# Kernel optimization log

Measured on AMD Instinct MI355X. Metric: run time of the kernel, lower is better.

## Reference

```python
import jax, jax.numpy as jnp
import numpy as np

EPS = 1e-5
HEADS, DK, DV = 8, 32, 64  # active_num_heads, active_key_dim, key_dim*attn_ratio


def _bn(x, g, b, m, v):
    # eval-mode BatchNorm2d over channel axis 1
    s = g * jax.lax.rsqrt(v + EPS)
    return x * s[None, :, None, None] + (b - m * s)[None, :, None, None]


def _bn_params(key, n):
    k1, k2, k3, k4 = jax.random.split(key, 4)
    gamma = 1.0 + 0.1 * jax.random.normal(k1, (n,), jnp.float32)
    beta = 0.1 * jax.random.normal(k2, (n,), jnp.float32)
    mean = 0.1 * jax.random.normal(k3, (n,), jnp.float32)
    var = jax.random.uniform(k4, (n,), jnp.float32, 0.5, 1.5)
    return gamma, beta, mean, var


def setup_inputs() -> dict:
    key = jax.random.key(0)
    ks = jax.random.split(key, 9)
    B, C, H, W = 8, 384, 32, 32
    Cqk, Cv = DK * HEADS, DV * HEADS  # 256, 512
    x = jax.random.normal(ks[0], (B, C, H, W), jnp.float32)
    w_q = jax.random.normal(ks[1], (Cqk, C), jnp.float32) / np.sqrt(C)
    w_k = jax.random.normal(ks[2], (Cqk, C), jnp.float32) / np.sqrt(C)
    w_v = jax.random.normal(ks[3], (Cv, C), jnp.float32) / np.sqrt(C)
    w_proj = jax.random.normal(ks[4], (C, Cv), jnp.float32) / np.sqrt(Cv)
    g_q, b_q, m_q, var_q = _bn_params(ks[5], Cqk)
    g_k, b_k, m_k, var_k = _bn_params(ks[6], Cqk)
    g_v, b_v, m_v, var_v = _bn_params(ks[7], Cv)
    g_p, b_p, m_p, var_p = _bn_params(ks[8], C)
    return dict(x=x, w_q=w_q, g_q=g_q, b_q=b_q, m_q=m_q, var_q=var_q,
                w_k=w_k, g_k=g_k, b_k=b_k, m_k=m_k, var_k=var_k,
                w_v=w_v, g_v=g_v, b_v=b_v, m_v=m_v, var_v=var_v,
                w_proj=w_proj, g_p=g_p, b_p=b_p, m_p=m_p, var_p=var_p)


def reference(x, w_q, g_q, b_q, m_q, var_q,
              w_k, g_k, b_k, m_k, var_k,
              w_v, g_v, b_v, m_v, var_v,
              w_proj, g_p, b_p, m_p, var_p):
    B, C, H, W = x.shape
    N = H * W
    # active config == max config, so dynamic index gathers are identity
    q = _bn(jnp.einsum('oc,bchw->bohw', w_q, x), g_q, b_q, m_q, var_q)
    k = _bn(jnp.einsum('oc,bchw->bohw', w_k, x), g_k, b_k, m_k, var_k)
    v = _bn(jnp.einsum('oc,bchw->bohw', w_v, x), g_v, b_v, m_v, var_v)
    q = q.reshape(B, HEADS, DK, N).transpose(0, 1, 3, 2)   # b h n d
    k = k.reshape(B, HEADS, DK, N)                          # b h d m
    v = v.reshape(B, HEADS, DV, N).transpose(0, 1, 3, 2)   # b h m e
    # NOTE: original forward does NOT apply self.scale
    attn = jax.nn.softmax(jnp.einsum('bhnd,bhdm->bhnm', q, k), axis=-1)
    out = jnp.einsum('bhnm,bhme->bhne', attn, v)
    out = out.transpose(0, 1, 3, 2).reshape(B, HEADS * DV, H, W)
    out = jax.nn.relu(out)
    out = _bn(jnp.einsum('oc,bchw->bohw', w_proj, out), g_p, b_p, m_p, var_p)
    return out
```

## Files before the change

### kernel.cpp

```cpp
#include <hip/hip_runtime.h>
#include <hip/hip_bf16.h>

#define DEVI __device__ __forceinline__

typedef __attribute__((ext_vector_type(8))) short s16x8;
typedef __attribute__((ext_vector_type(4))) short s16x4;
typedef __attribute__((ext_vector_type(4))) float f32x4;

#define LOG2E 1.4426950408889634f

DEVI short f2bs(float f) {
    unsigned u = __builtin_bit_cast(unsigned, f);
    unsigned r = (u + 0x7fffu + ((u >> 16) & 1u)) >> 16;
    return (short)r;
}

DEVI f32x4 mfma16(s16x8 a, s16x8 b, f32x4 c) {
    return __builtin_amdgcn_mfma_f32_16x16x32_bf16(a, b, c, 0, 0, 0);
}

DEVI void gl_lds16(const short* g, short* l) {
    __builtin_amdgcn_global_load_lds(
        (const __attribute__((address_space(1))) unsigned*)(const void*)g,
        (__attribute__((address_space(3))) unsigned*)(void*)l, 16, 0, 0);
}

__global__ __launch_bounds__(256) void k_prep_x(const float* __restrict__ x,
                                                short* __restrict__ xt) {
    __shared__ float tile[32][33];
    const int ct = blockIdx.x, nt = blockIdx.y, b = blockIdx.z;
    const int t = threadIdx.x;
    {
        const int j = t & 31, i0 = (t >> 5) * 4;
        const float* src = x + ((size_t)b * 384 + (size_t)ct * 32) * 1024 + nt * 32;
#pragma unroll
        for (int ii = 0; ii < 4; ++ii)
            tile[i0 + ii][j] = src[(size_t)(i0 + ii) * 1024 + j];
    }
    __syncthreads();
    {
        const int ii = t & 31, j0 = (t >> 5) * 4;
        short* dst = xt + ((size_t)b * 1024 + (size_t)nt * 32) * 384 + ct * 32;
#pragma unroll
        for (int jj = 0; jj < 4; ++jj)
            dst[(size_t)(j0 + jj) * 384 + ii] = f2bs(tile[ii][j0 + jj]);
    }
}

__global__ __launch_bounds__(256) void k_prep_w(
    const float* __restrict__ wq, const float* __restrict__ wk,
    const float* __restrict__ wv, const float* __restrict__ wp,
    short* __restrict__ wqkv, short* __restrict__ wpb,
    const float* gq, const float* bq, const float* mq, const float* vq,
    const float* gk, const float* bk, const float* mk, const float* vk,
    const float* gv, const float* bv, const float* mv, const float* vv,
    const float* gp, const float* bp, const float* mp, const float* vp,
    float* s_qkv, float* t_qkv, float* s_p, float* t_p) {
    int i = blockIdx.x * 256 + threadIdx.x;
    if (i < 1024) {
        const float *g, *bb, *mm, *vv_;
        int o = i;
        float post = 1.0f;
        if (i < 256)      { g = gq; bb = bq; mm = mq; vv_ = vq; post = LOG2E; }
        else if (i < 512) { g = gk; bb = bk; mm = mk; vv_ = vk; o = i - 256; }
        else              { g = gv; bb = bv; mm = mv; vv_ = vv; o = i - 512; }
        float s = g[o] * rsqrtf(vv_[o] + 1e-5f);
        s_qkv[i] = s * post;
        t_qkv[i] = (bb[o] - mm[o] * s) * post;
        if (i < 384) {
            float sp = gp[i] * rsqrtf(vp[i] + 1e-5f);
            s_p[i] = sp;
            t_p[i] = bp[i] - mp[i] * sp;
        }
    }
    const int NQKV = 1024 * 384;
    if (i < NQKV) {
        int o = i / 384;
        float v;
        if (o < 256)      v = wq[i];
        else if (o < 512) v = wk[i - 256 * 384];
        else              v = wv[i - 512 * 384];
        wqkv[i] = f2bs(v);
    } else {
        int j = i - NQKV;
        if (j < 384 * 512) wpb[j] = f2bs(wp[j]);
    }
}

__global__ __launch_bounds__(256, 2) void k_gemm_qkv(
    const short* __restrict__ wqkv, const short* __restrict__ xt,
    const float* __restrict__ s_qkv, const float* __restrict__ t_qkv,
    short* __restrict__ Qw, short* __restrict__ Kw, short* __restrict__ Vw) {
    __shared__ short AB[2][8192];
    const int t = threadIdx.x, lane = t & 63, w = t >> 6;
    const int g = lane >> 4, l15 = lane & 15;
    const int wr = w >> 1, wc = w & 1;
    const int jb = blockIdx.x, mb = blockIdx.y;

    const int cr = t >> 2, cu = t & 3;
    const int cperm = 8 * (cu ^ (cr & 3));
    const short* gA0 = wqkv + (size_t)(mb * 128 + cr) * 384 + cperm;
    const short* gA1 = wqkv + (size_t)(mb * 128 + cr + 64) * 384 + cperm;
    const short* gB0 = xt + (size_t)((size_t)jb * 128 + cr) * 384 + cperm;
    const short* gB1 = xt + (size_t)((size_t)jb * 128 + cr + 64) * 384 + cperm;

    f32x4 acc[4][4];
#pragma unroll
    for (int mi = 0; mi < 4; ++mi)
#pragma unroll
        for (int ni = 0; ni < 4; ++ni) acc[mi][ni] = f32x4{0.f, 0.f, 0.f, 0.f};

    const int kcol = 8 * (g ^ (l15 & 3));

    auto stage = [&](int ks, int buf) {
        short* base = AB[buf];
        gl_lds16(gA0 + ks * 32, base + t * 8);
        gl_lds16(gA1 + ks * 32, base + (t + 256) * 8);
        gl_lds16(gB0 + ks * 32, base + 4096 + t * 8);
        gl_lds16(gB1 + ks * 32, base + 4096 + (t + 256) * 8);
    };

    stage(0, 0);
    __syncthreads();

    for (int ks = 0; ks < 12; ++ks) {
        if (ks < 11) stage(ks + 1, (ks + 1) & 1);
        const short* base = AB[ks & 1];
        s16x8 a[4], b[4];
#pragma unroll
        for (int mi = 0; mi < 4; ++mi)
            a[mi] = *(const s16x8*)(base + (64 * wr + 16 * mi + l15) * 32 + kcol);
#pragma unroll
        for (int ni = 0; ni < 4; ++ni)
            b[ni] = *(const s16x8*)(base + 4096 + (64 * wc + 16 * ni + l15) * 32 + kcol);
#pragma unroll
        for (int mi = 0; mi < 4; ++mi)
#pragma unroll
            for (int ni = 0; ni < 4; ++ni)
                acc[mi][ni] = mfma16(a[mi], b[ni], acc[mi][ni]);
        __syncthreads();
    }

    const int m_base = mb * 128 + 64 * wr;
    const int j_base = jb * 128 + 64 * wc;
#pragma unroll
    for (int mi = 0; mi < 4; ++mi) {
        const int o0 = m_base + 16 * mi;
#pragma unroll
        for (int ni = 0; ni < 4; ++ni) {
            const int j = j_base + 16 * ni + l15;
            const int bb = j >> 10, n = j & 1023;
            if (o0 < 512) {
                const int o = o0 + 4 * g;
                const int isK = o0 >= 256;
                const int o2 = o - (isK ? 256 : 0);
                const int h = o2 >> 5, d0 = o2 & 31;
                s16x4 ov;
#pragma unroll
                for (int r = 0; r < 4; ++r)
                    ov[r] = f2bs(acc[mi][ni][r] * s_qkv[o + r] + t_qkv[o + r]);
                short* dst = (isK ? Kw : Qw) + (((size_t)bb * 8 + h) * 1024 + n) * 32 + d0;
                *(s16x4*)dst = ov;
            } else {
#pragma unroll
                for (int r = 0; r < 4; ++r) {
                    const int o = o0 + 4 * g + r;
                    float val = acc[mi][ni][r] * s_qkv[o] + t_qkv[o];
                    const int o2 = o - 512;
                    const int h = o2 >> 6, e = o2 & 63;
                    Vw[(((size_t)bb * 8 + h) * 64 + e) * 1024 + n] = f2bs(val);
                }
            }
        }
    }
}

__global__ __launch_bounds__(256, 2) void k_attn(const short* __restrict__ Qw,
                                                 const short* __restrict__ Kw,
                                                 const short* __restrict__ Vw,
                                                 short* __restrict__ Ow) {
    __shared__ short KV[2][6144];
    const int t = threadIdx.x, lane = t & 63, w = t >> 6;
    const int g = lane >> 4, l15 = lane & 15;
    const int low3 = blockIdx.x & 7;
    const int mid = blockIdx.x >> 3;
    const int rb = mid & 7;
    const int bh = ((mid >> 3) << 3) | low3;
    const int n_base = rb * 128 + w * 32;
    const short* Qb = Qw + (size_t)bh * (1024 * 32);
    const short* Kb = Kw + (size_t)bh * (1024 * 32);
    const short* Vb = Vw + (size_t)bh * (64 * 1024);

    s16x8 qf[2];
#pragma unroll
    for (int i = 0; i < 2; ++i)
        qf[i] = *(const s16x8*)(Qb + (size_t)(n_base + 16 * i + l15) * 32 + 8 * g);

    const int skr = t >> 2, sku = t & 3;
    const short* gK = Kb + (size_t)skr * 32 + 8 * (sku ^ (skr & 3));
    const int v0r = t >> 3, vu = t & 7;
    const short* gV0 = Vb + (size_t)v0r * 1024 + 8 * (vu ^ (v0r & 7));
    const short* gV1 = Vb + (size_t)(v0r + 32) * 1024 + 8 * (vu ^ ((v0r + 32) & 7));

    f32x4 oacc[2][4];
#pragma unroll
    for (int niq = 0; niq < 2; ++niq)
#pragma unroll
        for (int ei = 0; ei < 4; ++ei) oacc[niq][ei] = f32x4{0.f, 0.f, 0.f, 0.f};
    float l_part[2] = {0.f, 0.f};

    const int krow = 8 * (l15 >> 2) + (l15 & 3);
    const int kcol = 8 * (g ^ (l15 & 3));

    auto stage = [&](int m0, int buf) {
        short* base = KV[buf];
        gl_lds16(gK + m0 * 32, base + t * 8);
        gl_lds16(gV0 + m0, base + 2048 + t * 8);
        gl_lds16(gV1 + m0, base + 2048 + (t + 256) * 8);
    };

    stage(0, 0);
    __syncthreads();

    for (int mt = 0; mt < 16; ++mt) {
        if (mt < 15) stage((mt + 1) * 64, (mt + 1) & 1);
        const short* base = KV[mt & 1];
        s16x8 kf[4];
        kf[0] = *(const s16x8*)(base + (krow + 0) * 32 + kcol);
        kf[1] = *(const s16x8*)(base + (krow + 4) * 32 + kcol);
        kf[2] = *(const s16x8*)(base + (krow + 32) * 32 + kcol);
        kf[3] = *(const s16x8*)(base + (krow + 36) * 32 + kcol);
        s16x8 vb[2][4];
#pragma unroll
        for (int ki = 0; ki < 2; ++ki)
#pragma unroll
            for (int ei = 0; ei < 4; ++ei) {
                const int row = 16 * ei + l15;
                vb[ki][ei] = *(const s16x8*)(base + 2048 + row * 64 +
                                             8 * ((4 * ki + g) ^ (row & 7)));
            }
        f32x4 st[4][2];
#pragma unroll
        for (int mik = 0; mik < 4; ++mik)
#pragma unroll
            for (int niq = 0; niq < 2; ++niq)
                st[mik][niq] = mfma16(kf[mik], qf[niq], f32x4{0.f, 0.f, 0.f, 0.f});
        s16x4 pk[4][2];
#pragma unroll
        for (int mik = 0; mik < 4; ++mik)
#pragma unroll
            for (int niq = 0; niq < 2; ++niq) {
                float p[4];
#pragma unroll
                for (int r = 0; r < 4; ++r) p[r] = __builtin_amdgcn_exp2f(st[mik][niq][r]);
                l_part[niq] += (p[0] + p[1]) + (p[2] + p[3]);
#pragma unroll
                for (int r = 0; r < 4; ++r) pk[mik][niq][r] = f2bs(p[r]);
            }
#pragma unroll
        for (int ki = 0; ki < 2; ++ki)
#pragma unroll
            for (int niq = 0; niq < 2; ++niq) {
                s16x8 pb = __builtin_shufflevector(pk[2 * ki][niq], pk[2 * ki + 1][niq],
                                                   0, 1, 2, 3, 4, 5, 6, 7);
#pragma unroll
                for (int ei = 0; ei < 4; ++ei)
                    oacc[niq][ei] = mfma16(vb[ki][ei], pb, oacc[niq][ei]);
            }
        __syncthreads();
    }

    float li[2];
#pragma unroll
    for (int niq = 0; niq < 2; ++niq) {
        float s = l_part[niq];
        s += __shfl_xor(s, 16, 64);
        s += __shfl_xor(s, 32, 64);
        li[niq] = __builtin_amdgcn_rcpf(s);
    }
    const int b = bh >> 3, h = bh & 7;
#pragma unroll
    for (int niq = 0; niq < 2; ++niq) {
        const int n = n_base + 16 * niq + l15;
#pragma unroll
        for (int ei = 0; ei < 4; ++ei) {
            s16x4 ov;
#pragma unroll
            for (int r = 0; r < 4; ++r)
                ov[r] = f2bs(fmaxf(oacc[niq][ei][r] * li[niq], 0.f));
            *(s16x4*)(Ow + ((size_t)b * 1024 + n) * 512 + h * 64 + 16 * ei + 4 * g) = ov;
        }
    }
}

__global__ __launch_bounds__(256, 3) void k_proj(const short* __restrict__ wpb,
                                                 const short* __restrict__ Ow,
                                                 const float* __restrict__ s_p,
                                                 const float* __restrict__ t_p,
                                                 float* __restrict__ out) {
    __shared__ short AB[2][4096];
    const int t = threadIdx.x, lane = t & 63, w = t >> 6;
    const int g = lane >> 4, l15 = lane & 15;
    const int wr = w >> 1, wc = w & 1;
    const int jb = blockIdx.x, mb = blockIdx.y;

    const int cr = t >> 2, cu = t & 3;
    const int cperm = 8 * (cu ^ (cr & 3));
    const short* gA = wpb + (size_t)(mb * 64 + cr) * 512 + cperm;
    const short* gB = Ow + (size_t)((size_t)jb * 64 + cr) * 512 + cperm;

    f32x4 acc[2][2];
#pragma unroll
    for (int mi = 0; mi < 2; ++mi)
#pragma unroll
        for (int ni = 0; ni < 2; ++ni) acc[mi][ni] = f32x4{0.f, 0.f, 0.f, 0.f};

    const int kcol = 8 * (g ^ (l15 & 3));

    auto stage = [&](int ks, int buf) {
        short* base = AB[buf];
        gl_lds16(gA + ks * 32, base + t * 8);
        gl_lds16(gB + ks * 32, base + 2048 + t * 8);
    };

    stage(0, 0);
    __syncthreads();

    for (int ks = 0; ks < 16; ++ks) {
        if (ks < 15) stage(ks + 1, (ks + 1) & 1);
        const short* base = AB[ks & 1];
        s16x8 a[2], b[2];
#pragma unroll
        for (int mi = 0; mi < 2; ++mi)
            a[mi] = *(const s16x8*)(base + (32 * wr + 16 * mi + l15) * 32 + kcol);
#pragma unroll
        for (int ni = 0; ni < 2; ++ni)
            b[ni] = *(const s16x8*)(base + 2048 + (32 * wc + 16 * ni + l15) * 32 + kcol);
#pragma unroll
        for (int mi = 0; mi < 2; ++mi)
#pragma unroll
            for (int ni = 0; ni < 2; ++ni)
                acc[mi][ni] = mfma16(a[mi], b[ni], acc[mi][ni]);
        __syncthreads();
    }

    const int m_base = mb * 64 + 32 * wr;
    const int j_base = jb * 64 + 32 * wc;
#pragma unroll
    for (int mi = 0; mi < 2; ++mi) {
#pragma unroll
        for (int ni = 0; ni < 2; ++ni) {
            const int j = j_base + 16 * ni + l15;
            const int bb = j >> 10, n = j & 1023;
#pragma unroll
            for (int r = 0; r < 4; ++r) {
                const int c = m_base + 16 * mi + 4 * g + r;
                float v = acc[mi][ni][r] * s_p[c] + t_p[c];
                out[((size_t)bb * 384 + c) * 1024 + n] = v;
            }
        }
    }
}

extern "C" void kernel_launch(void* const* d_in, const int* in_sizes, int n_in,
                              void* d_out, int out_size, void* d_ws, size_t ws_size,
                              hipStream_t stream) {
    const float* x  = (const float*)d_in[0];
    const float* wq = (const float*)d_in[1];
    const float* gq = (const float*)d_in[2];
    const float* bq = (const float*)d_in[3];
    const float* mq = (const float*)d_in[4];
    const float* vq = (const float*)d_in[5];
    const float* wk = (const float*)d_in[6];
    const float* gk = (const float*)d_in[7];
    const float* bk = (const float*)d_in[8];
    const float* mk = (const float*)d_in[9];
    const float* vk = (const float*)d_in[10];
    const float* wv = (const float*)d_in[11];
    const float* gv = (const float*)d_in[12];
    const float* bv = (const float*)d_in[13];
    const float* mv = (const float*)d_in[14];
    const float* vv = (const float*)d_in[15];
    const float* wp = (const float*)d_in[16];
    const float* gp = (const float*)d_in[17];
    const float* bp = (const float*)d_in[18];
    const float* mp = (const float*)d_in[19];
    const float* vp = (const float*)d_in[20];
    float* out = (float*)d_out;

    char* ws = (char*)d_ws;
    size_t off = 0;
    auto alloc = [&](size_t bytes) {
        char* p = ws + off;
        off += (bytes + 255) & ~(size_t)255;
        return p;
    };
    short* xt    = (short*)alloc((size_t)8 * 1024 * 384 * 2);
    short* wqkv  = (short*)alloc((size_t)1024 * 384 * 2);
    short* wpb   = (short*)alloc((size_t)384 * 512 * 2);
    float* s_qkv = (float*)alloc(1024 * 4);
    float* t_qkv = (float*)alloc(1024 * 4);
    float* s_p   = (float*)alloc(384 * 4);
    float* t_p   = (float*)alloc(384 * 4);
    short* Qw    = (short*)alloc((size_t)8 * 8 * 1024 * 32 * 2);
    short* Kw    = (short*)alloc((size_t)8 * 8 * 1024 * 32 * 2);
    short* Vw    = (short*)alloc((size_t)8 * 8 * 64 * 1024 * 2);
    short* Ow    = (short*)alloc((size_t)8 * 1024 * 512 * 2);
    (void)ws_size; (void)in_sizes; (void)n_in; (void)out_size;

    k_prep_x<<<dim3(12, 32, 8), 256, 0, stream>>>(x, xt);
    k_prep_w<<<dim3((1024 * 384 + 384 * 512 + 255) / 256), 256, 0, stream>>>(
        wq, wk, wv, wp, wqkv, wpb,
        gq, bq, mq, vq, gk, bk, mk, vk, gv, bv, mv, vv, gp, bp, mp, vp,
        s_qkv, t_qkv, s_p, t_p);
    k_gemm_qkv<<<dim3(64, 8), 256, 0, stream>>>(wqkv, xt, s_qkv, t_qkv, Qw, Kw, Vw);
    k_attn<<<dim3(512), 256, 0, stream>>>(Qw, Kw, Vw, Ow);
    k_proj<<<dim3(128, 6), 256, 0, stream>>>(wpb, Ow, s_p, t_p, out);
}
```

Measured before the change: 58.80 us.

## Merge prep kernels, double K-tile depth in GEMMs and attention, add setprio

The two prep kernels become one launch, with block ranges split between the x transpose and the weight/BN-fold work, which saves one launch. The QKV and projection GEMMs now stage 64-wide K tiles with an 8-way XOR swizzle, and attention stages 128 keys per tile. Both halve the number of barrier-separated iterations at the cost of double the LDS per block. Attention also raises wave priority around its MFMA sections with s_setprio. The larger LDS footprint may reduce occupancy.

```diff
diff --git a/kernel.cpp b/kernel.cpp
--- a/kernel.cpp
+++ b/kernel.cpp
@@ -25,29 +25,8 @@
         (__attribute__((address_space(3))) unsigned*)(void*)l, 16, 0, 0);
 }
 
-__global__ __launch_bounds__(256) void k_prep_x(const float* __restrict__ x,
-                                                short* __restrict__ xt) {
-    __shared__ float tile[32][33];
-    const int ct = blockIdx.x, nt = blockIdx.y, b = blockIdx.z;
-    const int t = threadIdx.x;
-    {
-        const int j = t & 31, i0 = (t >> 5) * 4;
-        const float* src = x + ((size_t)b * 384 + (size_t)ct * 32) * 1024 + nt * 32;
-#pragma unroll
-        for (int ii = 0; ii < 4; ++ii)
-            tile[i0 + ii][j] = src[(size_t)(i0 + ii) * 1024 + j];
-    }
-    __syncthreads();
-    {
-        const int ii = t & 31, j0 = (t >> 5) * 4;
-        short* dst = xt + ((size_t)b * 1024 + (size_t)nt * 32) * 384 + ct * 32;
-#pragma unroll
-        for (int jj = 0; jj < 4; ++jj)
-            dst[(size_t)(j0 + jj) * 384 + ii] = f2bs(tile[ii][j0 + jj]);
-    }
-}
-
-__global__ __launch_bounds__(256) void k_prep_w(
+__global__ __launch_bounds__(256) void k_prep(
+    const float* __restrict__ x, short* __restrict__ xt,
     const float* __restrict__ wq, const float* __restrict__ wk,
     const float* __restrict__ wv, const float* __restrict__ wp,
     short* __restrict__ wqkv, short* __restrict__ wpb,
@@ -56,7 +35,29 @@
     const float* gv, const float* bv, const float* mv, const float* vv,
     const float* gp, const float* bp, const float* mp, const float* vp,
     float* s_qkv, float* t_qkv, float* s_p, float* t_p) {
-    int i = blockIdx.x * 256 + threadIdx.x;
+    __shared__ float tile[32][33];
+    const int bid = blockIdx.x;
+    const int t = threadIdx.x;
+    if (bid < 3072) {
+        const int ct = bid % 12, nt = (bid / 12) % 32, b = bid / 384;
+        {
+            const int j = t & 31, i0 = (t >> 5) * 4;
+            const float* src = x + ((size_t)b * 384 + (size_t)ct * 32) * 1024 + nt * 32;
+#pragma unroll
+            for (int ii = 0; ii < 4; ++ii)
+                tile[i0 + ii][j] = src[(size_t)(i0 + ii) * 1024 + j];
+        }
+        __syncthreads();
+        {
+            const int ii = t & 31, j0 = (t >> 5) * 4;
+            short* dst = xt + ((size_t)b * 1024 + (size_t)nt * 32) * 384 + ct * 32;
+#pragma unroll
+            for (int jj = 0; jj < 4; ++jj)
+                dst[(size_t)(j0 + jj) * 384 + ii] = f2bs(tile[ii][j0 + jj]);
+        }
+        return;
+    }
+    int i = (bid - 3072) * 256 + t;
     if (i < 1024) {
         const float *g, *bb, *mm, *vv_;
         int o = i;
@@ -91,18 +92,16 @@
     const short* __restrict__ wqkv, const short* __restrict__ xt,
     const float* __restrict__ s_qkv, const float* __restrict__ t_qkv,
     short* __restrict__ Qw, short* __restrict__ Kw, short* __restrict__ Vw) {
-    __shared__ short AB[2][8192];
+    __shared__ short AB[2][16384];
     const int t = threadIdx.x, lane = t & 63, w = t >> 6;
     const int g = lane >> 4, l15 = lane & 15;
     const int wr = w >> 1, wc = w & 1;
     const int jb = blockIdx.x, mb = blockIdx.y;
 
-    const int cr = t >> 2, cu = t & 3;
-    const int cperm = 8 * (cu ^ (cr & 3));
-    const short* gA0 = wqkv + (size_t)(mb * 128 + cr) * 384 + cperm;
-    const short* gA1 = wqkv + (size_t)(mb * 128 + cr + 64) * 384 + cperm;
-    const short* gB0 = xt + (size_t)((size_t)jb * 128 + cr) * 384 + cperm;
-    const short* gB1 = xt + (size_t)((size_t)jb * 128 + cr + 64) * 384 + cperm;
+    const int ar = t >> 3, au = t & 7;
+    const int aperm = 8 * (au ^ (ar & 7));
+    const short* gA = wqkv + (size_t)(mb * 128 + ar) * 384 + aperm;
+    const short* gB = xt + (size_t)((size_t)jb * 128 + ar) * 384 + aperm;
 
     f32x4 acc[4][4];
 #pragma unroll
@@ -110,34 +109,37 @@
 #pragma unroll
         for (int ni = 0; ni < 4; ++ni) acc[mi][ni] = f32x4{0.f, 0.f, 0.f, 0.f};
 
-    const int kcol = 8 * (g ^ (l15 & 3));
-
-    auto stage = [&](int ks, int buf) {
+    auto stage = [&](int kt, int buf) {
         short* base = AB[buf];
-        gl_lds16(gA0 + ks * 32, base + t * 8);
-        gl_lds16(gA1 + ks * 32, base + (t + 256) * 8);
-        gl_lds16(gB0 + ks * 32, base + 4096 + t * 8);
-        gl_lds16(gB1 + ks * 32, base + 4096 + (t + 256) * 8);
+#pragma unroll
+        for (int jj = 0; jj < 4; ++jj) {
+            gl_lds16(gA + (size_t)(32 * jj) * 384 + kt * 64, base + t * 8 + jj * 2048);
+            gl_lds16(gB + (size_t)(32 * jj) * 384 + kt * 64, base + 8192 + t * 8 + jj * 2048);
+        }
     };
 
     stage(0, 0);
     __syncthreads();
 
-    for (int ks = 0; ks < 12; ++ks) {
-        if (ks < 11) stage(ks + 1, (ks + 1) & 1);
-        const short* base = AB[ks & 1];
-        s16x8 a[4], b[4];
-#pragma unroll
-        for (int mi = 0; mi < 4; ++mi)
-            a[mi] = *(const s16x8*)(base + (64 * wr + 16 * mi + l15) * 32 + kcol);
-#pragma unroll
-        for (int ni = 0; ni < 4; ++ni)
-            b[ni] = *(const s16x8*)(base + 4096 + (64 * wc + 16 * ni + l15) * 32 + kcol);
-#pragma unroll
-        for (int mi = 0; mi < 4; ++mi)
+    for (int kt = 0; kt < 6; ++kt) {
+        if (kt < 5) stage(kt + 1, (kt + 1) & 1);
+        const short* base = AB[kt & 1];
+#pragma unroll
+        for (int ksub = 0; ksub < 2; ++ksub) {
+            const int kc = 8 * ((4 * ksub + g) ^ (l15 & 7));
+            s16x8 a[4], b[4];
+#pragma unroll
+            for (int mi = 0; mi < 4; ++mi)
+                a[mi] = *(const s16x8*)(base + (64 * wr + 16 * mi + l15) * 64 + kc);
 #pragma unroll
             for (int ni = 0; ni < 4; ++ni)
-                acc[mi][ni] = mfma16(a[mi], b[ni], acc[mi][ni]);
+                b[ni] = *(const s16x8*)(base + 8192 + (64 * wc + 16 * ni + l15) * 64 + kc);
+#pragma unroll
+            for (int mi = 0; mi < 4; ++mi)
+#pragma unroll
+                for (int ni = 0; ni < 4; ++ni)
+                    acc[mi][ni] = mfma16(a[mi], b[ni], acc[mi][ni]);
+        }
         __syncthreads();
     }
 
@@ -179,7 +181,7 @@
                                                  const short* __restrict__ Kw,
                                                  const short* __restrict__ Vw,
                                                  short* __restrict__ Ow) {
-    __shared__ short KV[2][6144];
+    __shared__ short KV[2][12288];
     const int t = threadIdx.x, lane = t & 63, w = t >> 6;
     const int g = lane >> 4, l15 = lane & 15;
     const int low3 = blockIdx.x & 7;
@@ -198,9 +200,8 @@
 
     const int skr = t >> 2, sku = t & 3;
     const short* gK = Kb + (size_t)skr * 32 + 8 * (sku ^ (skr & 3));
-    const int v0r = t >> 3, vu = t & 7;
-    const short* gV0 = Vb + (size_t)v0r * 1024 + 8 * (vu ^ (v0r & 7));
-    const short* gV1 = Vb + (size_t)(v0r + 32) * 1024 + 8 * (vu ^ ((v0r + 32) & 7));
+    const int vr = t >> 4, vu = t & 15;
+    const short* gV = Vb + (size_t)vr * 1024 + 8 * (vu ^ (vr & 7));
 
     f32x4 oacc[2][4];
 #pragma unroll
@@ -215,58 +216,68 @@
     auto stage = [&](int m0, int buf) {
         short* base = KV[buf];
         gl_lds16(gK + m0 * 32, base + t * 8);
-        gl_lds16(gV0 + m0, base + 2048 + t * 8);
-        gl_lds16(gV1 + m0, base + 2048 + (t + 256) * 8);
+        gl_lds16(gK + (m0 + 64) * 32, base + (t + 256) * 8);
+#pragma unroll
+        for (int jj = 0; jj < 4; ++jj)
+            gl_lds16(gV + (size_t)(16 * jj) * 1024 + m0, base + 4096 + t * 8 + jj * 2048);
     };
 
     stage(0, 0);
     __syncthreads();
 
-    for (int mt = 0; mt < 16; ++mt) {
-        if (mt < 15) stage((mt + 1) * 64, (mt + 1) & 1);
+    for (int mt = 0; mt < 8; ++mt) {
+        if (mt < 7) stage((mt + 1) * 128, (mt + 1) & 1);
         const short* base = KV[mt & 1];
-        s16x8 kf[4];
-        kf[0] = *(const s16x8*)(base + (krow + 0) * 32 + kcol);
-        kf[1] = *(const s16x8*)(base + (krow + 4) * 32 + kcol);
-        kf[2] = *(const s16x8*)(base + (krow + 32) * 32 + kcol);
-        kf[3] = *(const s16x8*)(base + (krow + 36) * 32 + kcol);
-        s16x8 vb[2][4];
-#pragma unroll
-        for (int ki = 0; ki < 2; ++ki)
-#pragma unroll
-            for (int ei = 0; ei < 4; ++ei) {
-                const int row = 16 * ei + l15;
-                vb[ki][ei] = *(const s16x8*)(base + 2048 + row * 64 +
-                                             8 * ((4 * ki + g) ^ (row & 7)));
-            }
-        f32x4 st[4][2];
-#pragma unroll
-        for (int mik = 0; mik < 4; ++mik)
-#pragma unroll
-            for (int niq = 0; niq < 2; ++niq)
-                st[mik][niq] = mfma16(kf[mik], qf[niq], f32x4{0.f, 0.f, 0.f, 0.f});
-        s16x4 pk[4][2];
-#pragma unroll
-        for (int mik = 0; mik < 4; ++mik)
-#pragma unroll
-            for (int niq = 0; niq < 2; ++niq) {
-                float p[4];
-#pragma unroll
-                for (int r = 0; r < 4; ++r) p[r] = __builtin_amdgcn_exp2f(st[mik][niq][r]);
-                l_part[niq] += (p[0] + p[1]) + (p[2] + p[3]);
-#pragma unroll
-                for (int r = 0; r < 4; ++r) pk[mik][niq][r] = f2bs(p[r]);
-            }
-#pragma unroll
-        for (int ki = 0; ki < 2; ++ki)
-#pragma unroll
-            for (int niq = 0; niq < 2; ++niq) {
-                s16x8 pb = __builtin_shufflevector(pk[2 * ki][niq], pk[2 * ki + 1][niq],
-                                                   0, 1, 2, 3, 4, 5, 6, 7);
-#pragma unroll
-                for (int ei = 0; ei < 4; ++ei)
-                    oacc[niq][ei] = mfma16(vb[ki][ei], pb, oacc[niq][ei]);
-            }
+#pragma unroll
+        for (int msub = 0; msub < 2; ++msub) {
+            const int mofs = 64 * msub;
+            s16x8 kf[4];
+            kf[0] = *(const s16x8*)(base + (krow + mofs + 0) * 32 + kcol);
+            kf[1] = *(const s16x8*)(base + (krow + mofs + 4) * 32 + kcol);
+            kf[2] = *(const s16x8*)(base + (krow + mofs + 32) * 32 + kcol);
+            kf[3] = *(const s16x8*)(base + (krow + mofs + 36) * 32 + kcol);
+            s16x8 vb[2][4];
+#pragma unroll
+            for (int ki = 0; ki < 2; ++ki)
+#pragma unroll
+                for (int ei = 0; ei < 4; ++ei) {
+                    const int row = 16 * ei + l15;
+                    vb[ki][ei] = *(const s16x8*)(base + 4096 + row * 128 +
+                                                 8 * ((8 * msub + 4 * ki + g) ^ (row & 7)));
+                }
+            __builtin_amdgcn_s_setprio(1);
+            f32x4 st[4][2];
+#pragma unroll
+            for (int mik = 0; mik < 4; ++mik)
+#pragma unroll
+                for (int niq = 0; niq < 2; ++niq)
+                    st[mik][niq] = mfma16(kf[mik], qf[niq], f32x4{0.f, 0.f, 0.f, 0.f});
+            __builtin_amdgcn_s_setprio(0);
+            s16x4 pk[4][2];
+#pragma unroll
+            for (int mik = 0; mik < 4; ++mik)
+#pragma unroll
+                for (int niq = 0; niq < 2; ++niq) {
+                    float p[4];
+#pragma unroll
+                    for (int r = 0; r < 4; ++r) p[r] = __builtin_amdgcn_exp2f(st[mik][niq][r]);
+                    l_part[niq] += (p[0] + p[1]) + (p[2] + p[3]);
+#pragma unroll
+                    for (int r = 0; r < 4; ++r) pk[mik][niq][r] = f2bs(p[r]);
+                }
+            __builtin_amdgcn_s_setprio(1);
+#pragma unroll
+            for (int ki = 0; ki < 2; ++ki)
+#pragma unroll
+                for (int niq = 0; niq < 2; ++niq) {
+                    s16x8 pb = __builtin_shufflevector(pk[2 * ki][niq], pk[2 * ki + 1][niq],
+                                                       0, 1, 2, 3, 4, 5, 6, 7);
+#pragma unroll
+                    for (int ei = 0; ei < 4; ++ei)
+                        oacc[niq][ei] = mfma16(vb[ki][ei], pb, oacc[niq][ei]);
+                }
+            __builtin_amdgcn_s_setprio(0);
+        }
         __syncthreads();
     }
 
@@ -298,16 +309,16 @@
                                                  const float* __restrict__ s_p,
                                                  const float* __restrict__ t_p,
                                                  float* __restrict__ out) {
-    __shared__ short AB[2][4096];
+    __shared__ short AB[2][8192];
     const int t = threadIdx.x, lane = t & 63, w = t >> 6;
     const int g = lane >> 4, l15 = lane & 15;
     const int wr = w >> 1, wc = w & 1;
     const int jb = blockIdx.x, mb = blockIdx.y;
 
-    const int cr = t >> 2, cu = t & 3;
-    const int cperm = 8 * (cu ^ (cr & 3));
-    const short* gA = wpb + (size_t)(mb * 64 + cr) * 512 + cperm;
-    const short* gB = Ow + (size_t)((size_t)jb * 64 + cr) * 512 + cperm;
+    const int ar = t >> 3, au = t & 7;
+    const int aperm = 8 * (au ^ (ar & 7));
+    const short* gA = wpb + (size_t)(mb * 64 + ar) * 512 + aperm;
+    const short* gB = Ow + (size_t)((size_t)jb * 64 + ar) * 512 + aperm;
 
     f32x4 acc[2][2];
 #pragma unroll
@@ -315,32 +326,37 @@
 #pragma unroll
         for (int ni = 0; ni < 2; ++ni) acc[mi][ni] = f32x4{0.f, 0.f, 0.f, 0.f};
 
-    const int kcol = 8 * (g ^ (l15 & 3));
-
-    auto stage = [&](int ks, int buf) {
+    auto stage = [&](int kt, int buf) {
         short* base = AB[buf];
-        gl_lds16(gA + ks * 32, base + t * 8);
-        gl_lds16(gB + ks * 32, base + 2048 + t * 8);
+#pragma unroll
+        for (int jj = 0; jj < 2; ++jj) {
+            gl_lds16(gA + (size_t)(32 * jj) * 512 + kt * 64, base + t * 8 + jj * 2048);
+            gl_lds16(gB + (size_t)(32 * jj) * 512 + kt * 64, base + 4096 + t * 8 + jj * 2048);
+        }
     };
 
     stage(0, 0);
     __syncthreads();
 
-    for (int ks = 0; ks < 16; ++ks) {
-        if (ks < 15) stage(ks + 1, (ks + 1) & 1);
-        const short* base = AB[ks & 1];
-        s16x8 a[2], b[2];
-#pragma unroll
-        for (int mi = 0; mi < 2; ++mi)
-            a[mi] = *(const s16x8*)(base + (32 * wr + 16 * mi + l15) * 32 + kcol);
-#pragma unroll
-        for (int ni = 0; ni < 2; ++ni)
-            b[ni] = *(const s16x8*)(base + 2048 + (32 * wc + 16 * ni + l15) * 32 + kcol);
-#pragma unroll
-        for (int mi = 0; mi < 2; ++mi)
+    for (int kt = 0; kt < 8; ++kt) {
+        if (kt < 7) stage(kt + 1, (kt + 1) & 1);
+        const short* base = AB[kt & 1];
+#pragma unroll
+        for (int ksub = 0; ksub < 2; ++ksub) {
+            const int kc = 8 * ((4 * ksub + g) ^ (l15 & 7));
+            s16x8 a[2], b[2];
+#pragma unroll
+            for (int mi = 0; mi < 2; ++mi)
+                a[mi] = *(const s16x8*)(base + (32 * wr + 16 * mi + l15) * 64 + kc);
 #pragma unroll
             for (int ni = 0; ni < 2; ++ni)
-                acc[mi][ni] = mfma16(a[mi], b[ni], acc[mi][ni]);
+                b[ni] = *(const s16x8*)(base + 4096 + (32 * wc + 16 * ni + l15) * 64 + kc);
+#pragma unroll
+            for (int mi = 0; mi < 2; ++mi)
+#pragma unroll
+                for (int ni = 0; ni < 2; ++ni)
+                    acc[mi][ni] = mfma16(a[mi], b[ni], acc[mi][ni]);
+        }
         __syncthreads();
     }
 
@@ -408,9 +424,8 @@
     short* Ow    = (short*)alloc((size_t)8 * 1024 * 512 * 2);
     (void)ws_size; (void)in_sizes; (void)n_in; (void)out_size;
 
-    k_prep_x<<<dim3(12, 32, 8), 256, 0, stream>>>(x, xt);
-    k_prep_w<<<dim3((1024 * 384 + 384 * 512 + 255) / 256), 256, 0, stream>>>(
-        wq, wk, wv, wp, wqkv, wpb,
+    k_prep<<<dim3(3072 + 2304), 256, 0, stream>>>(
+        x, xt, wq, wk, wv, wp, wqkv, wpb,
         gq, bq, mq, vq, gk, bk, mk, vk, gv, bv, mv, vv, gp, bp, mp, vp,
         s_qkv, t_qkv, s_p, t_p);
     k_gemm_qkv<<<dim3(64, 8), 256, 0, stream>>>(wqkv, xt, s_qkv, t_qkv, Qw, Kw, Vw);
```

New measurement: 53.74 us. 1.09x faster.
